# Kernel tuning notes

Hardware: AMD Instinct MI355X
Metric: run time of the kernel (lower is better)

## Reference

```python
import jax, jax.numpy as jnp
import numpy as np

B = 1024       # batch of triples
E = 50000      # num_entities
R = 500        # num_relations
D = 512        # dimension
P = 16         # parts
C = 8          # num_cores
ALPHA = 2.0    # -> q = alpha/2 = 1.0
Q = ALPHA / 2.0
DP = D // P    # 32


def setup_inputs() -> dict:
    key = jax.random.key(0)
    ks = jax.random.split(key, 10)
    xav_e = (2.0 / (E + D)) ** 0.5
    xav_r = (2.0 / (R + D)) ** 0.5
    return {
        "heads": jax.random.randint(ks[0], (B,), 0, E),
        "relations": jax.random.randint(ks[1], (B,), 0, R),
        "tails": jax.random.randint(ks[2], (B,), 0, E),
        "entity_w": jax.random.normal(ks[3], (E, D), dtype=jnp.float32) * xav_e,
        "relation_w": jax.random.normal(ks[4], (R, D), dtype=jnp.float32) * xav_r,
        "W_cores": jax.random.uniform(ks[5], (C, P, P, P), dtype=jnp.float32,
                                      minval=-0.01, maxval=0.01),
        "attn_w1": jax.random.normal(ks[6], (2 * D, D), dtype=jnp.float32) * (1.0 / (2 * D)) ** 0.5,
        "attn_b1": jnp.zeros((D,), dtype=jnp.float32),
        "attn_w2": jax.random.normal(ks[7], (D, C), dtype=jnp.float32) * (1.0 / D) ** 0.5,
        "attn_b2": jnp.zeros((C,), dtype=jnp.float32),
    }


def _pq_norm(x):
    # ((|x|^p).sum(2) ** q).sum(1), p=2
    return ((x * x).sum(2) ** Q).sum(1)


def _geometric_consistency(W_cores):
    # center of mass of |W| along each axis, per core; vectorized over cores
    coords = jnp.arange(P, dtype=jnp.float32)
    Wa = jnp.abs(W_cores)                      # [C,P,P,P]
    tot = Wa.sum(axis=(1, 2, 3))               # [C]
    cx = (Wa * coords[None, :, None, None]).sum(axis=(1, 2, 3)) / tot
    cy = (Wa * coords[None, None, :, None]).sum(axis=(1, 2, 3)) / tot
    cz = (Wa * coords[None, None, None, :]).sum(axis=(1, 2, 3)) / tot
    centers = jnp.stack([cx, cy, cz], axis=1)  # [C,3]
    d2 = ((centers[:, None, :] - centers[None, :, :]) ** 2).sum(-1)
    dist = jnp.sqrt(d2)
    masked = dist + jnp.eye(C, dtype=dist.dtype) * 1e6
    min_d = masked.min(axis=1)
    return -jnp.mean(jnp.log(min_d + 1e-6))


def reference(heads, relations, tails, entity_w, relation_w, W_cores,
              attn_w1, attn_b1, attn_w2, attn_b2):
    h = entity_w[heads]          # [B,D]
    r = relation_w[relations]    # [B,D]
    t = entity_w[tails]          # [B,D]

    hr = jnp.concatenate([h, r], axis=1)                       # [B,2D]
    hid = jax.nn.relu(hr @ attn_w1 + attn_b1)                  # [B,D]
    attn = jax.nn.softmax(hid @ attn_w2 + attn_b2, axis=1)     # [B,C]

    h3 = h.reshape(-1, DP, P)
    r3 = r.reshape(-1, DP, P)
    t3 = t.reshape(-1, DP, P)

    h_norm = _pq_norm(h3)
    r_norm = _pq_norm(r3)
    t_norm = _pq_norm(t3)

    # attention-weighted effective core per triple (sum over cores is linear,
    # so folding attn into W before the contraction is exactly the same math)
    Weff = jnp.einsum('bc,cpqs->bpqs', attn, W_cores)          # [B,P,P,P]

    # x1[b,i,s] = sum_{p,q} h[b,i,p] r[b,i,q] W[b,p,q,s]
    x1 = jnp.einsum('bip,biq,bpqs->bis', h3, r3, Weff)
    # x2[b,i,p] = sum_{q,s} r[b,i,q] t[b,i,s] W[b,p,q,s]
    x2 = jnp.einsum('biq,bis,bpqs->bip', r3, t3, Weff)
    # x3[b,i,q] = sum_{p,s} h[b,i,p] t[b,i,s] W[b,p,q,s]
    x3 = jnp.einsum('bip,bis,bpqs->biq', h3, t3, Weff)

    whr_norm = _pq_norm(x1)
    wrt_norm = _pq_norm(x2)
    wth_norm = _pq_norm(x3)

    scores = x1.reshape(-1, D) @ entity_w.T                    # [B,E]

    factor1 = jnp.mean(h_norm) + jnp.mean(r_norm) + jnp.mean(t_norm)
    factor2 = jnp.mean(whr_norm) + jnp.mean(wrt_norm) + jnp.mean(wth_norm)
    factor3 = _geometric_consistency(W_cores)
    return (scores, factor1, factor2, factor3, attn)
```

## Files before the change

kernel.cpp:

```cpp
#include <hip/hip_runtime.h>
#include <cstdint>
#include <cstddef>

#define NB 1024
#define NE 50000
#define DCOL 512
#define ATTN_C 8

static const size_t SCORES_OFF = (size_t)NB * NE;
static const size_t F1_OFF = SCORES_OFF + 0;
static const size_t F2_OFF = SCORES_OFF + 1;
static const size_t F3_OFF = SCORES_OFF + 2;
static const size_t ATTN_OFF = SCORES_OFF + 3;

typedef float f32x4 __attribute__((ext_vector_type(4)));
typedef short s16x8 __attribute__((ext_vector_type(8)));

__device__ __forceinline__ unsigned short f2bf(float f) {
  union { float f; uint32_t u; } x; x.f = f;
  uint32_t u = x.u;
  uint32_t r = (u + 0x7fffu + ((u >> 16) & 1u)) >> 16;
  return (unsigned short)r;
}

__device__ __forceinline__ void gload16(const void* g, void* l) {
  __builtin_amdgcn_global_load_lds(
      (const __attribute__((address_space(1))) uint32_t*)g,
      (__attribute__((address_space(3))) uint32_t*)l, 16, 0, 0);
}

__global__ __launch_bounds__(256)
void prep(const int* __restrict__ heads, const int* __restrict__ rels,
          const int* __restrict__ tails, const float* __restrict__ ew,
          const float* __restrict__ rw, const float* __restrict__ w1,
          unsigned short* __restrict__ hrb, unsigned short* __restrict__ w1t,
          float* __restrict__ n1) {
  int tid = threadIdx.x;
  if (blockIdx.x < NB) {
    int b = blockIdx.x;
    const float* h = ew + (size_t)heads[b] * DCOL;
    const float* r = rw + (size_t)rels[b] * DCOL;
    const float* t = ew + (size_t)tails[b] * DCOL;
    float acc = 0.f;
    #pragma unroll
    for (int it = 0; it < 2; ++it) {
      int d = it * 256 + tid;
      float hv = h[d], rv = r[d], tv = t[d];
      hrb[(size_t)b * 1024 + d] = f2bf(hv);
      hrb[(size_t)b * 1024 + DCOL + d] = f2bf(rv);
      acc += hv * hv + rv * rv + tv * tv;
    }
    __shared__ float red[256];
    red[tid] = acc; __syncthreads();
    for (int s = 128; s > 0; s >>= 1) {
      if (tid < s) red[tid] += red[tid + s];
      __syncthreads();
    }
    if (tid == 0) n1[b] = red[0];
  } else {
    int tb = blockIdx.x - NB;
    int nb = (tb & 15) * 32, kb = (tb >> 4) * 32;
    __shared__ float tile[32][33];
    int tx = tid & 31, ty = tid >> 5;
    #pragma unroll
    for (int rr = 0; rr < 32; rr += 8)
      tile[ty + rr][tx] = w1[(size_t)(kb + ty + rr) * 512 + nb + tx];
    __syncthreads();
    #pragma unroll
    for (int rr = 0; rr < 32; rr += 8)
      w1t[(size_t)(nb + ty + rr) * 1024 + kb + tx] = f2bf(tile[tx][ty + rr]);
  }
}

template <int EPI, int FR, int BF32>
__global__ __launch_bounds__(256, 2)
void gemm_nt(const unsigned short* __restrict__ A,
             const unsigned short* __restrict__ Bb,
             const float* __restrict__ Bf,
             float* __restrict__ C, const float* __restrict__ bias,
             int M, int N, int K, int Nc, int NrowsB) {
  constexpr int BM = FR * 32;
  constexpr int SMEM_A = BM * 128;
  __shared__ __align__(16) uint8_t smem[2 * SMEM_A];
  const int tid = threadIdx.x;
  const int lane = tid & 63;
  const int wv = tid >> 6;
  const int wm = wv >> 1, wn = wv & 1;
  const int m0 = blockIdx.x * BM;
  const int n0 = blockIdx.y * BM;
  const int rbytes = K * 2;

  f32x4 acc[FR][FR];
  #pragma unroll
  for (int i = 0; i < FR; ++i)
    #pragma unroll
    for (int j = 0; j < FR; ++j) acc[i][j] = (f32x4){0.f, 0.f, 0.f, 0.f};

  const int srow = lane >> 3;
  const int scol = lane & 7;
  const int nkt = K >> 6;

  for (int kt = 0; kt < nkt; ++kt) {
    #pragma unroll
    for (int j = 0; j < FR; ++j) {
      int chunk = wv * FR + j;
      int r = chunk * 8 + srow;
      int c = scol ^ (r & 7);
      const uint8_t* ga = (const uint8_t*)A + (size_t)(m0 + r) * rbytes + kt * 128 + c * 16;
      gload16(ga, &smem[chunk * 1024]);
      if (BF32) {
        int rn = n0 + r; rn = rn < NrowsB ? rn : NrowsB - 1;
        const float* src = Bf + (size_t)rn * K + kt * 64 + c * 8;
        float4 v0 = *(const float4*)src;
        float4 v1 = *(const float4*)(src + 4);
        s16x8 o;
        o[0] = (short)f2bf(v0.x); o[1] = (short)f2bf(v0.y);
        o[2] = (short)f2bf(v0.z); o[3] = (short)f2bf(v0.w);
        o[4] = (short)f2bf(v1.x); o[5] = (short)f2bf(v1.y);
        o[6] = (short)f2bf(v1.z); o[7] = (short)f2bf(v1.w);
        *(s16x8*)&smem[SMEM_A + chunk * 1024 + srow * 128 + scol * 16] = o;
      } else {
        const uint8_t* gb = (const uint8_t*)Bb + (size_t)(n0 + r) * rbytes + kt * 128 + c * 16;
        gload16(gb, &smem[SMEM_A + chunk * 1024]);
      }
    }
    __syncthreads();
    #pragma unroll
    for (int kk = 0; kk < 2; ++kk) {
      s16x8 af[FR], bfr[FR];
      #pragma unroll
      for (int f = 0; f < FR; ++f) {
        int ra = wm * 16 * FR + f * 16 + (lane & 15);
        int ca = (kk * 4 + (lane >> 4)) ^ (ra & 7);
        af[f] = *(const s16x8*)&smem[ra * 128 + ca * 16];
        int rb = wn * 16 * FR + f * 16 + (lane & 15);
        int cb = (kk * 4 + (lane >> 4)) ^ (rb & 7);
        bfr[f] = *(const s16x8*)&smem[SMEM_A + rb * 128 + cb * 16];
      }
      #pragma unroll
      for (int fm = 0; fm < FR; ++fm)
        #pragma unroll
        for (int fn = 0; fn < FR; ++fn)
          acc[fm][fn] = __builtin_amdgcn_mfma_f32_16x16x32_bf16(
              af[fm], bfr[fn], acc[fm][fn], 0, 0, 0);
    }
    __syncthreads();
  }

  const int rl = lane >> 4, cl = lane & 15;
  #pragma unroll
  for (int fm = 0; fm < FR; ++fm)
    #pragma unroll
    for (int fn = 0; fn < FR; ++fn)
      #pragma unroll
      for (int j = 0; j < 4; ++j) {
        int gm = m0 + wm * 16 * FR + fm * 16 + rl * 4 + j;
        int gn = n0 + wn * 16 * FR + fn * 16 + cl;
        if (gn < Nc) {
          float v = acc[fm][fn][j];
          if (EPI) v = fmaxf(v + bias[gn], 0.f);
          C[(size_t)gm * Nc + gn] = v;
        }
      }
}

__global__ __launch_bounds__(256, 2)
void triple_core(const int* __restrict__ heads, const int* __restrict__ rels,
                 const int* __restrict__ tails, const float* __restrict__ ew,
                 const float* __restrict__ rw, const float* __restrict__ wc,
                 const float* __restrict__ hid, const float* __restrict__ w2,
                 const float* __restrict__ b2, float* __restrict__ attn_out,
                 unsigned short* __restrict__ x1b, float* __restrict__ n2) {
  __shared__ float hs[512], rs[512], ts[512];
  __shared__ __align__(16) float W123[4096][4];
  __shared__ float att[8];
  __shared__ float wred[4][8];
  __shared__ float red[256];
  int b = blockIdx.x, tid = threadIdx.x;
  int lane = tid & 63, wid = tid >> 6;
  const float* hp_ = ew + (size_t)heads[b] * DCOL;
  const float* rp_ = rw + (size_t)rels[b] * DCOL;
  const float* tp_ = ew + (size_t)tails[b] * DCOL;
  float la[8] = {0, 0, 0, 0, 0, 0, 0, 0};
  #pragma unroll
  for (int it = 0; it < 2; ++it) {
    int d = it * 256 + tid;
    hs[d] = hp_[d]; rs[d] = rp_[d]; ts[d] = tp_[d];
    float hv = hid[(size_t)b * DCOL + d];
    #pragma unroll
    for (int c = 0; c < 8; ++c) la[c] = fmaf(hv, w2[d * 8 + c], la[c]);
  }
  #pragma unroll
  for (int off = 32; off > 0; off >>= 1)
    #pragma unroll
    for (int c = 0; c < 8; ++c) la[c] += __shfl_down(la[c], off);
  if (lane == 0)
    #pragma unroll
    for (int c = 0; c < 8; ++c) wred[wid][c] = la[c];
  __syncthreads();
  if (tid == 0) {
    float lg[8];
    #pragma unroll
    for (int c = 0; c < 8; ++c)
      lg[c] = wred[0][c] + wred[1][c] + wred[2][c] + wred[3][c] + b2[c];
    float mx = lg[0];
    #pragma unroll
    for (int c = 1; c < 8; ++c) mx = fmaxf(mx, lg[c]);
    float e[8], s = 0.f;
    #pragma unroll
    for (int c = 0; c < 8; ++c) { e[c] = expf(lg[c] - mx); s += e[c]; }
    #pragma unroll
    for (int c = 0; c < 8; ++c) {
      float a = e[c] / s;
      att[c] = a;
      attn_out[(size_t)b * 8 + c] = a;
    }
  }
  __syncthreads();
  #pragma unroll
  for (int it = 0; it < 16; ++it) {
    int idx = it * 256 + tid;
    float w = 0.f;
    #pragma unroll
    for (int c = 0; c < 8; ++c) w = fmaf(att[c], wc[c * 4096 + idx], w);
    int s = idx & 15, q = (idx >> 4) & 15, p = idx >> 8;
    W123[idx][0] = w;
    W123[(q * 16 + s) * 16 + p][1] = w;
    W123[(p * 16 + s) * 16 + q][2] = w;
  }
  __syncthreads();

  const int so = tid & 15;
  const int i0 = tid >> 4, i1 = i0 + 16;
  float h0[16], r0[16], t0[16], h1[16], r1[16], t1[16];
  #pragma unroll
  for (int k = 0; k < 16; ++k) {
    h0[k] = hs[i0 * 16 + k]; r0[k] = rs[i0 * 16 + k]; t0[k] = ts[i0 * 16 + k];
    h1[k] = hs[i1 * 16 + k]; r1[k] = rs[i1 * 16 + k]; t1[k] = ts[i1 * 16 + k];
  }
  float a10 = 0.f, a20 = 0.f, a30 = 0.f, a11 = 0.f, a21 = 0.f, a31 = 0.f;
  const float4* wp = (const float4*)&W123[so][0];
  #pragma unroll
  for (int u = 0; u < 16; ++u) {
    #pragma unroll
    for (int v = 0; v < 16; ++v) {
      float4 w = wp[u * 256 + v * 16];
      a10 = fmaf(h0[u] * r0[v], w.x, a10);
      a20 = fmaf(r0[u] * t0[v], w.y, a20);
      a30 = fmaf(h0[u] * t0[v], w.z, a30);
      a11 = fmaf(h1[u] * r1[v], w.x, a11);
      a21 = fmaf(r1[u] * t1[v], w.y, a21);
      a31 = fmaf(h1[u] * t1[v], w.z, a31);
    }
  }
  x1b[(size_t)b * 512 + i0 * 16 + so] = f2bf(a10);
  x1b[(size_t)b * 512 + i1 * 16 + so] = f2bf(a11);
  red[tid] = a10 * a10 + a20 * a20 + a30 * a30
           + a11 * a11 + a21 * a21 + a31 * a31;
  __syncthreads();
  for (int s = 128; s > 0; s >>= 1) {
    if (tid < s) red[tid] += red[tid + s];
    __syncthreads();
  }
  if (tid == 0) n2[b] = red[0];
}

__global__ __launch_bounds__(256)
void finalize(const float* __restrict__ n1, const float* __restrict__ n2,
              const float* __restrict__ wc, float* __restrict__ out) {
  int tid = threadIdx.x;
  __shared__ float red[256];
  float a = 0.f;
  for (int i = tid; i < NB; i += 256) a += n1[i];
  red[tid] = a; __syncthreads();
  for (int s = 128; s > 0; s >>= 1) { if (tid < s) red[tid] += red[tid + s]; __syncthreads(); }
  if (tid == 0) out[F1_OFF] = red[0] / (float)NB;
  __syncthreads();
  a = 0.f;
  for (int i = tid; i < NB; i += 256) a += n2[i];
  red[tid] = a; __syncthreads();
  for (int s = 128; s > 0; s >>= 1) { if (tid < s) red[tid] += red[tid + s]; __syncthreads(); }
  if (tid == 0) out[F2_OFF] = red[0] / (float)NB;
  __syncthreads();

  int c = tid >> 5, l = tid & 31;
  float tot = 0.f, cx = 0.f, cy = 0.f, cz = 0.f;
  for (int e = l; e < 4096; e += 32) {
    float w = fabsf(wc[c * 4096 + e]);
    int z = e & 15, y = (e >> 4) & 15, x = e >> 8;
    tot += w; cx += w * x; cy += w * y; cz += w * z;
  }
  #pragma unroll
  for (int off = 16; off > 0; off >>= 1) {
    tot += __shfl_down(tot, off);
    cx += __shfl_down(cx, off);
    cy += __shfl_down(cy, off);
    cz += __shfl_down(cz, off);
  }
  __shared__ float cent[8][3];
  if (l == 0) { cent[c][0] = cx / tot; cent[c][1] = cy / tot; cent[c][2] = cz / tot; }
  __syncthreads();
  if (tid == 0) {
    float f3 = 0.f;
    for (int i = 0; i < 8; ++i) {
      float mn = 1e30f;
      for (int j = 0; j < 8; ++j) {
        if (j == i) continue;
        float dx = cent[i][0] - cent[j][0];
        float dy = cent[i][1] - cent[j][1];
        float dz = cent[i][2] - cent[j][2];
        float d = sqrtf(dx * dx + dy * dy + dz * dz);
        mn = fminf(mn, d);
      }
      f3 += logf(mn + 1e-6f);
    }
    out[F3_OFF] = -f3 / 8.f;
  }
}

extern "C" void kernel_launch(void* const* d_in, const int* in_sizes, int n_in,
                              void* d_out, int out_size, void* d_ws, size_t ws_size,
                              hipStream_t stream) {
  const int* heads = (const int*)d_in[0];
  const int* rels = (const int*)d_in[1];
  const int* tails = (const int*)d_in[2];
  const float* ew = (const float*)d_in[3];
  const float* rw = (const float*)d_in[4];
  const float* wc = (const float*)d_in[5];
  const float* w1 = (const float*)d_in[6];
  const float* b1 = (const float*)d_in[7];
  const float* w2 = (const float*)d_in[8];
  const float* b2 = (const float*)d_in[9];
  float* out = (float*)d_out;

  uint8_t* ws = (uint8_t*)d_ws;
  unsigned short* hrb = (unsigned short*)ws;
  unsigned short* w1t = (unsigned short*)(ws + 2097152);
  float* hid = (float*)(ws + 2097152 + 1048576);
  unsigned short* x1b = (unsigned short*)(ws + 2097152 + 1048576 + 2097152);
  float* n1 = (float*)(ws + 2097152 + 1048576 + 2097152 + 1048576);
  float* n2 = n1 + NB;

  prep<<<NB + 512, 256, 0, stream>>>(heads, rels, tails, ew, rw, w1, hrb, w1t, n1);
  gemm_nt<1, 2, 0><<<dim3(16, 8), 256, 0, stream>>>(
      hrb, w1t, nullptr, hid, b1, 1024, 512, 1024, 512, 512);
  triple_core<<<NB, 256, 0, stream>>>(heads, rels, tails, ew, rw, wc,
                                      hid, w2, b2, out + ATTN_OFF, x1b, n2);
  gemm_nt<0, 4, 1><<<dim3(8, 391), 256, 0, stream>>>(
      x1b, nullptr, ew, out, nullptr, 1024, 50048, 512, NE, NE);
  finalize<<<1, 256, 0, stream>>>(n1, n2, wc, out);
}
```

Baseline: 254.6 us.

## Double-buffer GEMM K-loop with register prefetch and XCD-aware tile swizzle

Converts the NT GEMM to a double-buffered LDS pipeline. The next K-tile's global loads, including the fp32 entity rows kept in registers and converted to bf16 after the MFMAs, are issued before the current tile's math, which removes one barrier per iteration. It also switches to a 1D grid and, for the large scores GEMM, remaps block IDs so that each XCD handles a contiguous range of tiles, which should improve L2 reuse of the shared A/B tiles. The cost is doubled LDS use and more live registers, which may lower occupancy.

```diff
diff --git a/kernel.cpp b/kernel.cpp
--- a/kernel.cpp
+++ b/kernel.cpp
@@ -72,22 +72,32 @@
   }
 }
 
-template <int EPI, int FR, int BF32>
+template <int EPI, int FR, int BF32, int SWZ, int MT>
 __global__ __launch_bounds__(256, 2)
 void gemm_nt(const unsigned short* __restrict__ A,
              const unsigned short* __restrict__ Bb,
              const float* __restrict__ Bf,
              float* __restrict__ C, const float* __restrict__ bias,
-             int M, int N, int K, int Nc, int NrowsB) {
+             int K, int Nc, int NrowsB, int NT) {
   constexpr int BM = FR * 32;
-  constexpr int SMEM_A = BM * 128;
-  __shared__ __align__(16) uint8_t smem[2 * SMEM_A];
+  constexpr int TILE = BM * 128;
+  __shared__ __align__(16) uint8_t smem[4 * TILE];
   const int tid = threadIdx.x;
   const int lane = tid & 63;
   const int wv = tid >> 6;
   const int wm = wv >> 1, wn = wv & 1;
-  const int m0 = blockIdx.x * BM;
-  const int n0 = blockIdx.y * BM;
+
+  int m_t, n_t;
+  if (SWZ) {
+    int xcd = blockIdx.x & 7;
+    int l = blockIdx.x >> 3;
+    int w = xcd * ((MT * NT) >> 3) + l;
+    n_t = w / MT; m_t = w % MT;
+  } else {
+    m_t = blockIdx.x % MT; n_t = blockIdx.x / MT;
+  }
+  const int m0 = m_t * BM;
+  const int n0 = n_t * BM;
   const int rbytes = K * 2;
 
   f32x4 acc[FR][FR];
@@ -100,51 +110,98 @@
   const int scol = lane & 7;
   const int nkt = K >> 6;
 
+  float4 br0[FR], br1[FR];
+
+  #pragma unroll
+  for (int j = 0; j < FR; ++j) {
+    const int chunk = wv * FR + j;
+    const int r = chunk * 8 + srow;
+    const int c = scol ^ (r & 7);
+    gload16((const uint8_t*)A + (size_t)(m0 + r) * rbytes + c * 16,
+            &smem[chunk * 1024]);
+    if (BF32) {
+      int rn = n0 + r; rn = rn < NrowsB ? rn : NrowsB - 1;
+      const float* src = Bf + (size_t)rn * K + c * 8;
+      br0[j] = *(const float4*)src;
+      br1[j] = *(const float4*)(src + 4);
+    } else {
+      gload16((const uint8_t*)Bb + (size_t)(n0 + r) * rbytes + c * 16,
+              &smem[TILE + chunk * 1024]);
+    }
+  }
+  if (BF32) {
+    #pragma unroll
+    for (int j = 0; j < FR; ++j) {
+      const int chunk = wv * FR + j;
+      s16x8 o;
+      o[0] = (short)f2bf(br0[j].x); o[1] = (short)f2bf(br0[j].y);
+      o[2] = (short)f2bf(br0[j].z); o[3] = (short)f2bf(br0[j].w);
+      o[4] = (short)f2bf(br1[j].x); o[5] = (short)f2bf(br1[j].y);
+      o[6] = (short)f2bf(br1[j].z); o[7] = (short)f2bf(br1[j].w);
+      *(s16x8*)&smem[TILE + chunk * 1024 + srow * 128 + scol * 16] = o;
+    }
+  }
+  __syncthreads();
+
+  int cur = 0;
   for (int kt = 0; kt < nkt; ++kt) {
-    #pragma unroll
-    for (int j = 0; j < FR; ++j) {
-      int chunk = wv * FR + j;
-      int r = chunk * 8 + srow;
-      int c = scol ^ (r & 7);
-      const uint8_t* ga = (const uint8_t*)A + (size_t)(m0 + r) * rbytes + kt * 128 + c * 16;
-      gload16(ga, &smem[chunk * 1024]);
-      if (BF32) {
-        int rn = n0 + r; rn = rn < NrowsB ? rn : NrowsB - 1;
-        const float* src = Bf + (size_t)rn * K + kt * 64 + c * 8;
-        float4 v0 = *(const float4*)src;
-        float4 v1 = *(const float4*)(src + 4);
-        s16x8 o;
-        o[0] = (short)f2bf(v0.x); o[1] = (short)f2bf(v0.y);
-        o[2] = (short)f2bf(v0.z); o[3] = (short)f2bf(v0.w);
-        o[4] = (short)f2bf(v1.x); o[5] = (short)f2bf(v1.y);
-        o[6] = (short)f2bf(v1.z); o[7] = (short)f2bf(v1.w);
-        *(s16x8*)&smem[SMEM_A + chunk * 1024 + srow * 128 + scol * 16] = o;
-      } else {
-        const uint8_t* gb = (const uint8_t*)Bb + (size_t)(n0 + r) * rbytes + kt * 128 + c * 16;
-        gload16(gb, &smem[SMEM_A + chunk * 1024]);
+    const int nxt = cur ^ 1;
+    const bool hn = (kt + 1) < nkt;
+    if (hn) {
+      const int kn = kt + 1;
+      #pragma unroll
+      for (int j = 0; j < FR; ++j) {
+        const int chunk = wv * FR + j;
+        const int r = chunk * 8 + srow;
+        const int c = scol ^ (r & 7);
+        gload16((const uint8_t*)A + (size_t)(m0 + r) * rbytes + kn * 128 + c * 16,
+                &smem[nxt * 2 * TILE + chunk * 1024]);
+        if (BF32) {
+          int rn = n0 + r; rn = rn < NrowsB ? rn : NrowsB - 1;
+          const float* src = Bf + (size_t)rn * K + kn * 64 + c * 8;
+          br0[j] = *(const float4*)src;
+          br1[j] = *(const float4*)(src + 4);
+        } else {
+          gload16((const uint8_t*)Bb + (size_t)(n0 + r) * rbytes + kn * 128 + c * 16,
+                  &smem[nxt * 2 * TILE + TILE + chunk * 1024]);
+        }
       }
     }
-    __syncthreads();
+    const uint8_t* sa = &smem[cur * 2 * TILE];
+    const uint8_t* sb = &smem[cur * 2 * TILE + TILE];
     #pragma unroll
     for (int kk = 0; kk < 2; ++kk) {
-      s16x8 af[FR], bfr[FR];
+      s16x8 af[FR], bfv[FR];
       #pragma unroll
       for (int f = 0; f < FR; ++f) {
-        int ra = wm * 16 * FR + f * 16 + (lane & 15);
-        int ca = (kk * 4 + (lane >> 4)) ^ (ra & 7);
-        af[f] = *(const s16x8*)&smem[ra * 128 + ca * 16];
-        int rb = wn * 16 * FR + f * 16 + (lane & 15);
-        int cb = (kk * 4 + (lane >> 4)) ^ (rb & 7);
-        bfr[f] = *(const s16x8*)&smem[SMEM_A + rb * 128 + cb * 16];
+        const int ra = wm * 16 * FR + f * 16 + (lane & 15);
+        const int ca = (kk * 4 + (lane >> 4)) ^ (ra & 7);
+        af[f] = *(const s16x8*)&sa[ra * 128 + ca * 16];
+        const int rb = wn * 16 * FR + f * 16 + (lane & 15);
+        const int cb = (kk * 4 + (lane >> 4)) ^ (rb & 7);
+        bfv[f] = *(const s16x8*)&sb[rb * 128 + cb * 16];
       }
       #pragma unroll
       for (int fm = 0; fm < FR; ++fm)
         #pragma unroll
         for (int fn = 0; fn < FR; ++fn)
           acc[fm][fn] = __builtin_amdgcn_mfma_f32_16x16x32_bf16(
-              af[fm], bfr[fn], acc[fm][fn], 0, 0, 0);
+              af[fm], bfv[fn], acc[fm][fn], 0, 0, 0);
+    }
+    if (hn && BF32) {
+      #pragma unroll
+      for (int j = 0; j < FR; ++j) {
+        const int chunk = wv * FR + j;
+        s16x8 o;
+        o[0] = (short)f2bf(br0[j].x); o[1] = (short)f2bf(br0[j].y);
+        o[2] = (short)f2bf(br0[j].z); o[3] = (short)f2bf(br0[j].w);
+        o[4] = (short)f2bf(br1[j].x); o[5] = (short)f2bf(br1[j].y);
+        o[6] = (short)f2bf(br1[j].z); o[7] = (short)f2bf(br1[j].w);
+        *(s16x8*)&smem[nxt * 2 * TILE + TILE + chunk * 1024 + srow * 128 + scol * 16] = o;
+      }
     }
     __syncthreads();
+    cur = nxt;
   }
 
   const int rl = lane >> 4, cl = lane & 15;
@@ -342,11 +399,11 @@
   float* n2 = n1 + NB;
 
   prep<<<NB + 512, 256, 0, stream>>>(heads, rels, tails, ew, rw, w1, hrb, w1t, n1);
-  gemm_nt<1, 2, 0><<<dim3(16, 8), 256, 0, stream>>>(
-      hrb, w1t, nullptr, hid, b1, 1024, 512, 1024, 512, 512);
+  gemm_nt<1, 2, 0, 0, 16><<<128, 256, 0, stream>>>(
+      hrb, w1t, nullptr, hid, b1, 1024, 512, 512, 8);
   triple_core<<<NB, 256, 0, stream>>>(heads, rels, tails, ew, rw, wc,
                                       hid, w2, b2, out + ATTN_OFF, x1b, n2);
-  gemm_nt<0, 4, 1><<<dim3(8, 391), 256, 0, stream>>>(
-      x1b, nullptr, ew, out, nullptr, 1024, 50048, 512, NE, NE);
+  gemm_nt<0, 4, 1, 1, 8><<<3128, 256, 0, stream>>>(
+      x1b, nullptr, ew, out, nullptr, 512, NE, NE, 391);
   finalize<<<1, 256, 0, stream>>>(n1, n2, wc, out);
 }
```

After: 248.4 us. 1.02x faster.

## Pre-convert entity table to bf16 and double-buffer GEMM with XCD-aware tile swizzle

Applied to the files above, without the earlier changes.

The prep kernel now converts the whole entity embedding table to a padded bf16 copy, so the big scores GEMM can load both operands with direct global-to-LDS loads instead of converting fp32 in the inner loop. The GEMM is restructured into a two-stage double-buffered pipeline using explicit vmcnt waits and barriers, so loads for the next k-tile overlap with MFMA work on the current one. A 1D grid with an XCD-aware swizzle maps neighbouring tiles onto the same chiplet to improve L2 reuse of the shared operand. The trade-off is an extra full pass over the 100MB fp32 table to write about 51MB of bf16, and twice the LDS per block, which may reduce occupancy.

```diff
diff --git a/kernel.cpp b/kernel.cpp
--- a/kernel.cpp
+++ b/kernel.cpp
@@ -4,6 +4,7 @@
 
 #define NB 1024
 #define NE 50000
+#define NE_PAD 50048
 #define DCOL 512
 #define ATTN_C 8
 
@@ -29,12 +30,20 @@
       (__attribute__((address_space(3))) uint32_t*)l, 16, 0, 0);
 }
 
+template <int N>
+__device__ __forceinline__ void waitcnt_vm() {
+  static_assert(N == 0 || N == 4 || N == 8, "literal dispatch");
+  if constexpr (N == 0) asm volatile("s_waitcnt vmcnt(0)" ::: "memory");
+  else if constexpr (N == 4) asm volatile("s_waitcnt vmcnt(4)" ::: "memory");
+  else if constexpr (N == 8) asm volatile("s_waitcnt vmcnt(8)" ::: "memory");
+}
+
 __global__ __launch_bounds__(256)
 void prep(const int* __restrict__ heads, const int* __restrict__ rels,
           const int* __restrict__ tails, const float* __restrict__ ew,
           const float* __restrict__ rw, const float* __restrict__ w1,
           unsigned short* __restrict__ hrb, unsigned short* __restrict__ w1t,
-          float* __restrict__ n1) {
+          unsigned short* __restrict__ ewb, float* __restrict__ n1) {
   int tid = threadIdx.x;
   if (blockIdx.x < NB) {
     int b = blockIdx.x;
@@ -57,7 +66,7 @@
       __syncthreads();
     }
     if (tid == 0) n1[b] = red[0];
-  } else {
+  } else if (blockIdx.x < NB + 512) {
     int tb = blockIdx.x - NB;
     int nb = (tb & 15) * 32, kb = (tb >> 4) * 32;
     __shared__ float tile[32][33];
@@ -69,25 +78,49 @@
     #pragma unroll
     for (int rr = 0; rr < 32; rr += 8)
       w1t[(size_t)(nb + ty + rr) * 1024 + kb + tx] = f2bf(tile[tx][ty + rr]);
-  }
-}
-
-template <int EPI, int FR, int BF32>
+  } else {
+    const int n4valid = NE * DCOL / 4;
+    const int n4tot = NE_PAD * DCOL / 4;
+    int i = (blockIdx.x - NB - 512) * 256 + tid;
+    const int stride = 2048 * 256;
+    for (; i < n4tot; i += stride) {
+      float x = 0.f, y = 0.f, z = 0.f, w = 0.f;
+      if (i < n4valid) {
+        float4 v = ((const float4*)ew)[i];
+        x = v.x; y = v.y; z = v.z; w = v.w;
+      }
+      union { unsigned short u[4]; uint2 v2; } o;
+      o.u[0] = f2bf(x); o.u[1] = f2bf(y); o.u[2] = f2bf(z); o.u[3] = f2bf(w);
+      ((uint2*)ewb)[i] = o.v2;
+    }
+  }
+}
+
+template <int EPI, int FR, int SWZ, int MT>
 __global__ __launch_bounds__(256, 2)
 void gemm_nt(const unsigned short* __restrict__ A,
-             const unsigned short* __restrict__ Bb,
-             const float* __restrict__ Bf,
+             const unsigned short* __restrict__ B,
              float* __restrict__ C, const float* __restrict__ bias,
-             int M, int N, int K, int Nc, int NrowsB) {
+             int K, int Nc, int NT) {
   constexpr int BM = FR * 32;
-  constexpr int SMEM_A = BM * 128;
-  __shared__ __align__(16) uint8_t smem[2 * SMEM_A];
+  constexpr int TILE = BM * 128;
+  __shared__ __align__(16) uint8_t smem[4 * TILE];
   const int tid = threadIdx.x;
   const int lane = tid & 63;
   const int wv = tid >> 6;
   const int wm = wv >> 1, wn = wv & 1;
-  const int m0 = blockIdx.x * BM;
-  const int n0 = blockIdx.y * BM;
+
+  int m_t, n_t;
+  if (SWZ) {
+    int xcd = blockIdx.x & 7;
+    int l = blockIdx.x >> 3;
+    int w = xcd * ((MT * NT) >> 3) + l;
+    n_t = w / MT; m_t = w % MT;
+  } else {
+    m_t = blockIdx.x % MT; n_t = blockIdx.x / MT;
+  }
+  const int m0 = m_t * BM;
+  const int n0 = n_t * BM;
   const int rbytes = K * 2;
 
   f32x4 acc[FR][FR];
@@ -100,52 +133,61 @@
   const int scol = lane & 7;
   const int nkt = K >> 6;
 
-  for (int kt = 0; kt < nkt; ++kt) {
+  auto stage = [&](int kt, int buf) {
     #pragma unroll
     for (int j = 0; j < FR; ++j) {
-      int chunk = wv * FR + j;
-      int r = chunk * 8 + srow;
-      int c = scol ^ (r & 7);
-      const uint8_t* ga = (const uint8_t*)A + (size_t)(m0 + r) * rbytes + kt * 128 + c * 16;
-      gload16(ga, &smem[chunk * 1024]);
-      if (BF32) {
-        int rn = n0 + r; rn = rn < NrowsB ? rn : NrowsB - 1;
-        const float* src = Bf + (size_t)rn * K + kt * 64 + c * 8;
-        float4 v0 = *(const float4*)src;
-        float4 v1 = *(const float4*)(src + 4);
-        s16x8 o;
-        o[0] = (short)f2bf(v0.x); o[1] = (short)f2bf(v0.y);
-        o[2] = (short)f2bf(v0.z); o[3] = (short)f2bf(v0.w);
-        o[4] = (short)f2bf(v1.x); o[5] = (short)f2bf(v1.y);
-        o[6] = (short)f2bf(v1.z); o[7] = (short)f2bf(v1.w);
-        *(s16x8*)&smem[SMEM_A + chunk * 1024 + srow * 128 + scol * 16] = o;
-      } else {
-        const uint8_t* gb = (const uint8_t*)Bb + (size_t)(n0 + r) * rbytes + kt * 128 + c * 16;
-        gload16(gb, &smem[SMEM_A + chunk * 1024]);
-      }
-    }
-    __syncthreads();
+      const int chunk = wv * FR + j;
+      const int r = chunk * 8 + srow;
+      const int c = scol ^ (r & 7);
+      gload16((const uint8_t*)A + (size_t)(m0 + r) * rbytes + kt * 128 + c * 16,
+              &smem[buf * 2 * TILE + chunk * 1024]);
+      gload16((const uint8_t*)B + (size_t)(n0 + r) * rbytes + kt * 128 + c * 16,
+              &smem[buf * 2 * TILE + TILE + chunk * 1024]);
+    }
+  };
+  auto compute = [&](int buf) {
+    const uint8_t* sa = &smem[buf * 2 * TILE];
+    const uint8_t* sb = sa + TILE;
     #pragma unroll
     for (int kk = 0; kk < 2; ++kk) {
-      s16x8 af[FR], bfr[FR];
+      s16x8 af[FR], bfv[FR];
       #pragma unroll
       for (int f = 0; f < FR; ++f) {
-        int ra = wm * 16 * FR + f * 16 + (lane & 15);
-        int ca = (kk * 4 + (lane >> 4)) ^ (ra & 7);
-        af[f] = *(const s16x8*)&smem[ra * 128 + ca * 16];
-        int rb = wn * 16 * FR + f * 16 + (lane & 15);
-        int cb = (kk * 4 + (lane >> 4)) ^ (rb & 7);
-        bfr[f] = *(const s16x8*)&smem[SMEM_A + rb * 128 + cb * 16];
+        const int ra = wm * 16 * FR + f * 16 + (lane & 15);
+        const int ca = (kk * 4 + (lane >> 4)) ^ (ra & 7);
+        af[f] = *(const s16x8*)&sa[ra * 128 + ca * 16];
+        const int rb = wn * 16 * FR + f * 16 + (lane & 15);
+        const int cb = (kk * 4 + (lane >> 4)) ^ (rb & 7);
+        bfv[f] = *(const s16x8*)&sb[rb * 128 + cb * 16];
       }
       #pragma unroll
       for (int fm = 0; fm < FR; ++fm)
         #pragma unroll
         for (int fn = 0; fn < FR; ++fn)
           acc[fm][fn] = __builtin_amdgcn_mfma_f32_16x16x32_bf16(
-              af[fm], bfr[fn], acc[fm][fn], 0, 0, 0);
-    }
-    __syncthreads();
-  }
+              af[fm], bfv[fn], acc[fm][fn], 0, 0, 0);
+    }
+  };
+
+  stage(0, 0);
+  stage(1, 1);
+  for (int kt = 0; kt < nkt - 1; ++kt) {
+    const int cur = kt & 1;
+    waitcnt_vm<2 * FR>();
+    __builtin_amdgcn_sched_barrier(0);
+    __builtin_amdgcn_s_barrier();
+    __builtin_amdgcn_sched_barrier(0);
+    compute(cur);
+    __builtin_amdgcn_sched_barrier(0);
+    __builtin_amdgcn_s_barrier();
+    __builtin_amdgcn_sched_barrier(0);
+    if (kt + 2 < nkt) stage(kt + 2, cur);
+  }
+  waitcnt_vm<0>();
+  __builtin_amdgcn_sched_barrier(0);
+  __builtin_amdgcn_s_barrier();
+  __builtin_amdgcn_sched_barrier(0);
+  compute((nkt - 1) & 1);
 
   const int rl = lane >> 4, cl = lane & 15;
   #pragma unroll
@@ -334,19 +376,22 @@
   float* out = (float*)d_out;
 
   uint8_t* ws = (uint8_t*)d_ws;
-  unsigned short* hrb = (unsigned short*)ws;
-  unsigned short* w1t = (unsigned short*)(ws + 2097152);
-  float* hid = (float*)(ws + 2097152 + 1048576);
-  unsigned short* x1b = (unsigned short*)(ws + 2097152 + 1048576 + 2097152);
-  float* n1 = (float*)(ws + 2097152 + 1048576 + 2097152 + 1048576);
+  const size_t EWB_SZ = (size_t)NE_PAD * DCOL * 2;
+  unsigned short* ewb = (unsigned short*)ws;
+  unsigned short* hrb = (unsigned short*)(ws + EWB_SZ);
+  unsigned short* w1t = (unsigned short*)(ws + EWB_SZ + 2097152);
+  float* hid = (float*)(ws + EWB_SZ + 2097152 + 1048576);
+  unsigned short* x1b = (unsigned short*)(ws + EWB_SZ + 2097152 + 1048576 + 2097152);
+  float* n1 = (float*)(ws + EWB_SZ + 2097152 + 1048576 + 2097152 + 1048576);
   float* n2 = n1 + NB;
 
-  prep<<<NB + 512, 256, 0, stream>>>(heads, rels, tails, ew, rw, w1, hrb, w1t, n1);
-  gemm_nt<1, 2, 0><<<dim3(16, 8), 256, 0, stream>>>(
-      hrb, w1t, nullptr, hid, b1, 1024, 512, 1024, 512, 512);
+  prep<<<NB + 512 + 2048, 256, 0, stream>>>(heads, rels, tails, ew, rw, w1,
+                                            hrb, w1t, ewb, n1);
+  gemm_nt<1, 2, 0, 16><<<128, 256, 0, stream>>>(
+      hrb, w1t, hid, b1, 1024, 512, 8);
   triple_core<<<NB, 256, 0, stream>>>(heads, rels, tails, ew, rw, wc,
                                       hid, w2, b2, out + ATTN_OFF, x1b, n2);
-  gemm_nt<0, 4, 1><<<dim3(8, 391), 256, 0, stream>>>(
-      x1b, nullptr, ew, out, nullptr, 1024, 50048, 512, NE, NE);
+  gemm_nt<0, 4, 1, 8><<<3128, 256, 0, stream>>>(
+      x1b, ewb, out, nullptr, 512, NE, 391);
   finalize<<<1, 256, 0, stream>>>(n1, n2, wc, out);
 }
```

Result: faster. 212.3 us (-16.6%).
